# Kernel optimization log

Hardware: AMD Instinct MI355X
Metric: run time of the kernel (lower is better)

The kernel has to match this reference:

```python
import jax, jax.numpy as jnp
import numpy as np

EPS = 1e-12  # torch F.normalize eps
NUM_HEADS = 4
DT = 0.25
NUM_STEPS = 4


def _l2norm(x, axis=-1):
    n = jnp.sqrt(jnp.sum(x * x, axis=axis, keepdims=True))
    return x / jnp.maximum(n, EPS)


def setup_inputs() -> dict:
    key = jax.random.key(0)
    k0, k1, k2, k3, k4 = jax.random.split(key, 5)
    B, T, D = 4, 2048, 256
    z = jax.random.normal(k0, (B, T, D), dtype=jnp.float32)
    omega = jax.random.normal(k1, (1, 1, D), dtype=jnp.float32) * 0.1
    Wqk = jax.random.normal(k2, (2 * D, D), dtype=jnp.float32) * (1.0 / np.sqrt(D))
    Wout = jax.random.normal(k3, (D, D), dtype=jnp.float32) * (1.0 / np.sqrt(D))
    bout = jax.random.normal(k4, (D,), dtype=jnp.float32) * 0.01
    return {"z": z, "omega": omega, "Wqk": Wqk, "Wout": Wout, "bout": bout}


def _kuramoto(x, omega, Wqk, Wout, bout):
    # x: [B, T, D]
    B, T, D = x.shape
    hd = D // NUM_HEADS
    qk = x @ Wqk.T  # [B, T, 2D]
    q, k = jnp.split(qk, 2, axis=-1)
    q = _l2norm(q.reshape(B, T, NUM_HEADS, hd))  # cosine-normalized per head
    k = _l2norm(k.reshape(B, T, NUM_HEADS, hd))
    # coupling: [B, H, T, T] cosine similarity
    coupling = jnp.einsum("bqhd,bkhd->bhqk", q, k)
    # sin nonlinearity replaces softmax
    force = jnp.einsum("bhqk,bkhd->bqhd", jnp.sin(coupling), k).reshape(B, T, D)
    return omega + force @ Wout.T + bout


def reference(z, omega, Wqk, Wout, bout):
    def f(x):
        return _kuramoto(x, omega, Wqk, Wout, bout)

    x = z
    for _ in range(NUM_STEPS):
        x = _l2norm(x)
        k1 = f(x)
        k2 = f(x + DT / 2 * k1)
        k3 = f(x + DT / 2 * k2)
        k4 = f(x + DT * k3)
        x = x + DT / 6 * (k1 + 2 * k2 + 2 * k3 + k4)
    return _l2norm(x)
```

## Files before the change

### kernel.cpp

```cpp
#include <hip/hip_runtime.h>
#include <cmath>

#define NB 4
#define TT 2048
#define DD 256
#define NH 4
#define BT (NB*TT)

static constexpr float DT_ = 0.25f;

typedef _Float16 f16x8 __attribute__((ext_vector_type(8)));
typedef _Float16 f16x4 __attribute__((ext_vector_type(4)));
typedef float    f32x4 __attribute__((ext_vector_type(4)));

static constexpr size_t HSZ = (size_t)NB * NH * TT * 64;
static constexpr size_t FSZ = (size_t)BT * 256;

__device__ __forceinline__ void gload16(const void* g, void* l) {
    __builtin_amdgcn_global_load_lds(
        (const __attribute__((address_space(1))) void*)g,
        (__attribute__((address_space(3))) void*)l,
        16, 0, 0);
}

__global__ __launch_bounds__(256)
void split_weights(const float* __restrict__ Wqk, const float* __restrict__ Wout,
                   _Float16* __restrict__ WqkH, _Float16* __restrict__ WqkL,
                   _Float16* __restrict__ WoutH, _Float16* __restrict__ WoutL)
{
    const int idx = blockIdx.x * 256 + threadIdx.x;
    const float4 v = (idx < 32768) ? ((const float4*)Wqk)[idx]
                                   : ((const float4*)Wout)[idx - 32768];
    f16x4 h, l;
    h[0]=(_Float16)v.x; l[0]=(_Float16)(v.x-(float)h[0]);
    h[1]=(_Float16)v.y; l[1]=(_Float16)(v.y-(float)h[1]);
    h[2]=(_Float16)v.z; l[2]=(_Float16)(v.z-(float)h[2]);
    h[3]=(_Float16)v.w; l[3]=(_Float16)(v.w-(float)h[3]);
    if (idx < 32768) { ((f16x4*)WqkH)[idx] = h; ((f16x4*)WqkL)[idx] = l; }
    else { ((f16x4*)WoutH)[idx-32768] = h; ((f16x4*)WoutL)[idx-32768] = l; }
}

__global__ __launch_bounds__(256)
void comb_weights(const float* __restrict__ Wqk, const float* __restrict__ Wout,
                  const float* __restrict__ omega, const float* __restrict__ bout,
                  _Float16* __restrict__ WcombH, _Float16* __restrict__ WcombL,
                  float* __restrict__ qkob)
{
    __shared__ float qrow[256];
    __shared__ float pr[256];
    const int n = blockIdx.x;
    const int k = threadIdx.x;
    qrow[k] = Wqk[n * 256 + k];
    __syncthreads();
    float s = 0.f;
    for (int m = 0; m < 256; ++m) s = fmaf(qrow[m], Wout[m * 256 + k], s);
    const _Float16 h = (_Float16)s;
    WcombH[n * 256 + k] = h;
    WcombL[n * 256 + k] = (_Float16)(s - (float)h);
    pr[k] = (omega[k] + bout[k]) * qrow[k];
    __syncthreads();
    if (k == 0) {
        float t = 0.f;
        for (int i = 0; i < 256; ++i) t += pr[i];
        qkob[n] = t;
    }
}

__global__ __launch_bounds__(256)
void l2norm_rows(const float* __restrict__ src, float* __restrict__ dst,
                 _Float16* __restrict__ dstH, _Float16* __restrict__ dstL) {
    const int wave = threadIdx.x >> 6;
    const int lane = threadIdx.x & 63;
    const size_t row = (size_t)blockIdx.x * 4 + wave;
    float4 v = ((const float4*)(src + row * DD))[lane];
    float ss = v.x*v.x + v.y*v.y + v.z*v.z + v.w*v.w;
    #pragma unroll
    for (int off = 32; off; off >>= 1) ss += __shfl_xor(ss, off, 64);
    const float inv = 1.0f / fmaxf(sqrtf(ss), 1e-12f);
    v.x *= inv; v.y *= inv; v.z *= inv; v.w *= inv;
    ((float4*)(dst + row * DD))[lane] = v;
    if (dstH != nullptr) {
        f16x4 h, l;
        h[0]=(_Float16)v.x; l[0]=(_Float16)(v.x-(float)h[0]);
        h[1]=(_Float16)v.y; l[1]=(_Float16)(v.y-(float)h[1]);
        h[2]=(_Float16)v.z; l[2]=(_Float16)(v.z-(float)h[2]);
        h[3]=(_Float16)v.w; l[3]=(_Float16)(v.w-(float)h[3]);
        ((f16x4*)(dstH + row * DD))[lane] = h;
        ((f16x4*)(dstL + row * DD))[lane] = l;
    }
}

__global__ __launch_bounds__(256)
void reduce_F(const float* __restrict__ Fp, float* __restrict__ Facc,
              _Float16* __restrict__ SH, _Float16* __restrict__ SL, int faccm)
{
    const size_t idx = (size_t)blockIdx.x * 256 + threadIdx.x;
    const float4 a = ((const float4*)Fp)[idx];
    const float4 b = ((const float4*)(Fp + FSZ))[idx];
    const float4 c = ((const float4*)(Fp + 2*FSZ))[idx];
    float4 s = make_float4(a.x+b.x+c.x, a.y+b.y+c.y, a.z+b.z+c.z, a.w+b.w+c.w);
    if (faccm == 1) {
        ((float4*)Facc)[idx] = s;
    } else if (faccm == 2) {
        float4 f = ((const float4*)Facc)[idx];
        f.x += 2.f*s.x; f.y += 2.f*s.y; f.z += 2.f*s.z; f.w += 2.f*s.w;
        ((float4*)Facc)[idx] = f;
    } else {
        const float4 f = ((const float4*)Facc)[idx];
        s.x += f.x; s.y += f.y; s.z += f.z; s.w += f.w;
    }
    f16x4 h, l;
    h[0]=(_Float16)s.x; l[0]=(_Float16)(s.x-(float)h[0]);
    h[1]=(_Float16)s.y; l[1]=(_Float16)(s.y-(float)h[1]);
    h[2]=(_Float16)s.z; l[2]=(_Float16)(s.z-(float)h[2]);
    h[3]=(_Float16)s.w; l[3]=(_Float16)(s.w-(float)h[3]);
    ((f16x4*)SH)[idx] = h;
    ((f16x4*)SL)[idx] = l;
}

__global__ __launch_bounds__(256, 3)
void gemm_mfma(const _Float16* __restrict__ AH, const _Float16* __restrict__ AL,
               const _Float16* __restrict__ BH, const _Float16* __restrict__ BL,
               float* __restrict__ qkx, const float* __restrict__ qkob,
               const float* __restrict__ omega, const float* __restrict__ bout,
               const float* __restrict__ xin, float* __restrict__ xout,
               _Float16* __restrict__ Qhi, _Float16* __restrict__ Qlo,
               _Float16* __restrict__ Khi, _Float16* __restrict__ Klo,
               _Float16* __restrict__ KtrH,
               int mode, float cc)
{
    __shared__ _Float16 Ah[128 * 64];
    __shared__ _Float16 Al[128 * 64];
    __shared__ _Float16 Bh[64 * 64];
    __shared__ _Float16 Bl[64 * 64];
    const int m0 = blockIdx.x * 128, n0 = blockIdx.y * 64;
    const int t  = threadIdx.x;
    const int w  = t >> 6;
    const int l  = t & 63;
    const int lr = l & 15;
    const int lq = l >> 4;
    const int m7 = lr & 7;
    const int rr = l >> 3;
    const int cg = ((l & 7) ^ rr) * 8;

    f32x4 acc[2][4];
    #pragma unroll
    for (int s = 0; s < 2; ++s)
        #pragma unroll
        for (int nt = 0; nt < 4; ++nt) acc[s][nt] = (f32x4){0.f,0.f,0.f,0.f};

    for (int kc = 0; kc < 4; ++kc) {
        const int k0 = kc * 64;
        __syncthreads();
        #pragma unroll
        for (int a = 0; a < 4; ++a) {
            const int rg = 8*w + 32*a;
            gload16(AH + (size_t)(m0 + rg + rr) * 256 + k0 + cg, &Ah[rg * 64]);
            gload16(AL + (size_t)(m0 + rg + rr) * 256 + k0 + cg, &Al[rg * 64]);
            if (a < 2) {
                gload16(BH + (size_t)(n0 + rg + rr) * 256 + k0 + cg, &Bh[rg * 64]);
                gload16(BL + (size_t)(n0 + rg + rr) * 256 + k0 + cg, &Bl[rg * 64]);
            }
        }
        __syncthreads();
        #pragma unroll
        for (int c = 0; c < 2; ++c) {
            const int xo = (((4*c + lq) ^ m7) << 4);
            f16x8 ah[2], al[2], bh[4], bl[4];
            #pragma unroll
            for (int s = 0; s < 2; ++s) {
                ah[s] = *(const f16x8*)((const char*)Ah + (32*w + 16*s + lr) * 128 + xo);
                al[s] = *(const f16x8*)((const char*)Al + (32*w + 16*s + lr) * 128 + xo);
            }
            #pragma unroll
            for (int nt = 0; nt < 4; ++nt) {
                bh[nt] = *(const f16x8*)((const char*)Bh + (16*nt + lr) * 128 + xo);
                bl[nt] = *(const f16x8*)((const char*)Bl + (16*nt + lr) * 128 + xo);
            }
            #pragma unroll
            for (int s = 0; s < 2; ++s)
                #pragma unroll
                for (int nt = 0; nt < 4; ++nt) {
                    acc[s][nt] = __builtin_amdgcn_mfma_f32_16x16x32_f16(ah[s], bh[nt], acc[s][nt], 0, 0, 0);
                    acc[s][nt] = __builtin_amdgcn_mfma_f32_16x16x32_f16(ah[s], bl[nt], acc[s][nt], 0, 0, 0);
                    acc[s][nt] = __builtin_amdgcn_mfma_f32_16x16x32_f16(al[s], bh[nt], acc[s][nt], 0, 0, 0);
                }
        }
    }

    if (mode == 2) {
        #pragma unroll
        for (int s = 0; s < 2; ++s) {
            const int row0 = m0 + 32*w + 16*s + 4*lq;
            #pragma unroll
            for (int nt = 0; nt < 4; ++nt) {
                const int col = n0 + 16*nt + lr;
                const float ob = omega[col] + bout[col];
                #pragma unroll
                for (int r = 0; r < 4; ++r) {
                    const size_t off = (size_t)(row0 + r) * 256 + col;
                    xout[off] = xin[off] + (DT_ / 6.0f) * acc[s][nt][r] + DT_ * ob;
                }
            }
        }
    } else {
        float val[2][4][4];
        #pragma unroll
        for (int s = 0; s < 2; ++s) {
            const int row0 = m0 + 32*w + 16*s + 4*lq;
            #pragma unroll
            for (int nt = 0; nt < 4; ++nt) {
                const int col = n0 + 16*nt + lr;
                #pragma unroll
                for (int r = 0; r < 4; ++r) {
                    const size_t qo = (size_t)(row0 + r) * 512 + col;
                    if (mode == 0) {
                        val[s][nt][r] = acc[s][nt][r];
                        qkx[qo] = acc[s][nt][r];
                    } else {
                        val[s][nt][r] = qkx[qo] + cc * (acc[s][nt][r] + qkob[col]);
                    }
                }
            }
        }
        float ss[2][4];
        #pragma unroll
        for (int s = 0; s < 2; ++s)
            #pragma unroll
            for (int r = 0; r < 4; ++r) {
                float v = 0.f;
                #pragma unroll
                for (int nt = 0; nt < 4; ++nt) v += val[s][nt][r] * val[s][nt][r];
                ss[s][r] = v;
            }
        #pragma unroll
        for (int off = 1; off < 16; off <<= 1)
            #pragma unroll
            for (int s = 0; s < 2; ++s)
                #pragma unroll
                for (int r = 0; r < 4; ++r)
                    ss[s][r] += __shfl_xor(ss[s][r], off, 64);
        const int  b    = m0 >> 11;
        const int  h    = (n0 >> 6) & 3;
        const bool is_k = (n0 >= 256);
        const size_t bhi = (size_t)b * NH + h;
        _Float16* dhi = (is_k ? Khi : Qhi) + bhi * (size_t)TT * 64;
        _Float16* dlo = (is_k ? Klo : Qlo) + bhi * (size_t)TT * 64;
        const int mloc = m0 & (TT - 1);
        #pragma unroll
        for (int s = 0; s < 2; ++s) {
            const int r0 = 32*w + 16*s + 4*lq;
            float inv[4];
            #pragma unroll
            for (int r = 0; r < 4; ++r) inv[r] = 1.0f / fmaxf(sqrtf(ss[s][r]), 1e-12f);
            #pragma unroll
            for (int nt = 0; nt < 4; ++nt) {
                const int d = 16*nt + lr;
                f16x4 hv, lv;
                #pragma unroll
                for (int r = 0; r < 4; ++r) {
                    const float v2 = val[s][nt][r] * inv[r];
                    hv[r] = (_Float16)v2;
                    lv[r] = (_Float16)(v2 - (float)hv[r]);
                    dhi[(size_t)(mloc + r0 + r) * 64 + d] = hv[r];
                    dlo[(size_t)(mloc + r0 + r) * 64 + d] = lv[r];
                }
                if (is_k) {
                    const size_t tb = bhi * (size_t)64 * TT + (size_t)d * TT + mloc + r0;
                    *(f16x4*)(KtrH + tb) = hv;
                }
            }
        }
    }
}

__global__ __launch_bounds__(256, 4)
void kuramoto_attn(const _Float16* __restrict__ Qhi, const _Float16* __restrict__ Qlo,
                   const _Float16* __restrict__ Khi, const _Float16* __restrict__ Klo,
                   const _Float16* __restrict__ KtrH,
                   float* __restrict__ Fp)
{
    __shared__ _Float16 KjH[64 * 64];
    __shared__ _Float16 KjL[64 * 64];
    __shared__ _Float16 KdH[64 * 64];
    __shared__ _Float16 Pw[4][2][16 * 64];
    const int bh = blockIdx.z;
    const int b  = bh >> 2, h = bh & 3;
    const size_t base  = (size_t)bh * TT * 64;
    const size_t tbase = (size_t)bh * 64 * TT;
    const int t0 = blockIdx.y * 11;
    const int tn = (blockIdx.y == 2) ? 10 : 11;
    float* Fout = Fp + (size_t)blockIdx.y * FSZ;
    const int t = threadIdx.x;
    const int w = t >> 6;
    const int l = t & 63;
    const int lr = l & 15;
    const int lq = l >> 4;
    const int i0 = blockIdx.x * 128 + w * 32;
    const int m7 = lr & 7;
    const int x0 = ((lq ^ m7) << 4);
    const int x1 = (((lq + 4) ^ m7) << 4);
    const int rr = l >> 3;
    const int cg = ((l & 7) ^ rr) * 8;

    const _Float16* gKh = Khi  + base  + (size_t)(8*w + rr) * 64 + cg;
    const _Float16* gKl = Klo  + base  + (size_t)(8*w + rr) * 64 + cg;
    const _Float16* gKd = KtrH + tbase + (size_t)(8*w + rr) * TT + cg;
    _Float16* lKh = &KjH[(8*w) * 64];
    _Float16* lKl = &KjL[(8*w) * 64];
    _Float16* lKd = &KdH[(8*w) * 64];

    f16x8 qh[2][2], ql[2][2];
    #pragma unroll
    for (int s = 0; s < 2; ++s) {
        const size_t qoff = base + (size_t)(i0 + 16*s + lr) * 64 + lq * 8;
        qh[s][0] = *(const f16x8*)(Qhi + qoff);
        qh[s][1] = *(const f16x8*)(Qhi + qoff + 32);
        ql[s][0] = *(const f16x8*)(Qlo + qoff);
        ql[s][1] = *(const f16x8*)(Qlo + qoff + 32);
    }

    f32x4 Facc[2][4];
    #pragma unroll
    for (int s = 0; s < 2; ++s)
        #pragma unroll
        for (int nt = 0; nt < 4; ++nt) Facc[s][nt] = (f32x4){0.f, 0.f, 0.f, 0.f};

    for (int tt = 0; tt < tn; ++tt) {
        const int j0 = (t0 + tt) * 64;
        __syncthreads();
        gload16(gKh + (size_t)j0 * 64,           lKh);
        gload16(gKh + (size_t)j0 * 64 + 32 * 64, lKh + 32 * 64);
        gload16(gKl + (size_t)j0 * 64,           lKl);
        gload16(gKl + (size_t)j0 * 64 + 32 * 64, lKl + 32 * 64);
        gload16(gKd + j0,                        lKd);
        gload16(gKd + j0 + (size_t)32 * TT,      lKd + 32 * 64);
        __syncthreads();
        #pragma unroll
        for (int nt = 0; nt < 4; ++nt) {
            const int rb = (16*nt + lr) * 128;
            f16x8 kh0 = *(const f16x8*)((const char*)KjH + rb + x0);
            f16x8 kh1 = *(const f16x8*)((const char*)KjH + rb + x1);
            f16x8 kl0 = *(const f16x8*)((const char*)KjL + rb + x0);
            f16x8 kl1 = *(const f16x8*)((const char*)KjL + rb + x1);
            #pragma unroll
            for (int s = 0; s < 2; ++s) {
                f32x4 a = (f32x4){0.f, 0.f, 0.f, 0.f};
                __builtin_amdgcn_s_setprio(1);
                a = __builtin_amdgcn_mfma_f32_16x16x32_f16(kh0, qh[s][0], a, 0, 0, 0);
                a = __builtin_amdgcn_mfma_f32_16x16x32_f16(kh1, qh[s][1], a, 0, 0, 0);
                a = __builtin_amdgcn_mfma_f32_16x16x32_f16(kl0, qh[s][0], a, 0, 0, 0);
                a = __builtin_amdgcn_mfma_f32_16x16x32_f16(kl1, qh[s][1], a, 0, 0, 0);
                a = __builtin_amdgcn_mfma_f32_16x16x32_f16(kh0, ql[s][0], a, 0, 0, 0);
                a = __builtin_amdgcn_mfma_f32_16x16x32_f16(kh1, ql[s][1], a, 0, 0, 0);
                __builtin_amdgcn_s_setprio(0);
                f16x4 pv;
                #pragma unroll
                for (int r = 0; r < 4; ++r) pv[r] = (_Float16)__sinf(a[r]);
                *(f16x4*)((char*)&Pw[w][s][0] + lr * 128
                          + (((2*nt + (lq >> 1)) ^ m7) << 4) + ((lq & 1) << 3)) = pv;
            }
        }
        f16x8 ph[2][2];
        #pragma unroll
        for (int s = 0; s < 2; ++s) {
            ph[s][0] = *(const f16x8*)((const char*)&Pw[w][s][0] + lr * 128 + x0);
            ph[s][1] = *(const f16x8*)((const char*)&Pw[w][s][0] + lr * 128 + x1);
        }
        #pragma unroll
        for (int nt = 0; nt < 4; ++nt) {
            const int rb = (16*nt + lr) * 128;
            f16x8 kh0 = *(const f16x8*)((const char*)KdH + rb + x0);
            f16x8 kh1 = *(const f16x8*)((const char*)KdH + rb + x1);
            __builtin_amdgcn_s_setprio(1);
            #pragma unroll
            for (int s = 0; s < 2; ++s) {
                Facc[s][nt] = __builtin_amdgcn_mfma_f32_16x16x32_f16(ph[s][0], kh0, Facc[s][nt], 0, 0, 0);
                Facc[s][nt] = __builtin_amdgcn_mfma_f32_16x16x32_f16(ph[s][1], kh1, Facc[s][nt], 0, 0, 0);
            }
            __builtin_amdgcn_s_setprio(0);
        }
    }
    #pragma unroll
    for (int s = 0; s < 2; ++s) {
        float* fo = Fout + ((size_t)b * TT + i0 + 16*s + 4*lq) * 256 + h * 64 + lr;
        #pragma unroll
        for (int nt = 0; nt < 4; ++nt)
            #pragma unroll
            for (int r = 0; r < 4; ++r)
                fo[(size_t)r * 256 + nt * 16] = Facc[s][nt][r];
    }
}

extern "C" void kernel_launch(void* const* d_in, const int* in_sizes, int n_in,
                              void* d_out, int out_size, void* d_ws, size_t ws_size,
                              hipStream_t stream) {
    const float* z     = (const float*)d_in[0];
    const float* omega = (const float*)d_in[1];
    const float* Wqk   = (const float*)d_in[2];
    const float* Wout  = (const float*)d_in[3];
    const float* bout  = (const float*)d_in[4];

    float* x    = (float*)d_ws;
    float* Facc = x + FSZ;
    float* Fp   = Facc + FSZ;
    float* qkx  = Fp + 3 * FSZ;
    float* qkob = qkx + (size_t)BT * 512;
    _Float16* xsH  = (_Float16*)(qkob + 512);
    _Float16* xsL  = xsH  + FSZ;
    _Float16* Qhi  = xsL  + FSZ;
    _Float16* Qlo  = Qhi  + HSZ;
    _Float16* Khi  = Qlo  + HSZ;
    _Float16* Klo  = Khi  + HSZ;
    _Float16* KtrH = Klo  + HSZ;
    _Float16* WqkH = KtrH + HSZ;
    _Float16* WqkL = WqkH + (size_t)512 * 256;
    _Float16* WoutH= WqkL + (size_t)512 * 256;
    _Float16* WoutL= WoutH + (size_t)256 * 256;
    _Float16* WcombH = WoutL + (size_t)256 * 256;
    _Float16* WcombL = WcombH + (size_t)512 * 256;

    split_weights<<<192, 256, 0, stream>>>(Wqk, Wout, WqkH, WqkL, WoutH, WoutL);
    comb_weights<<<512, 256, 0, stream>>>(Wqk, Wout, omega, bout, WcombH, WcombL, qkob);

    for (int step = 0; step < 4; ++step) {
        l2norm_rows<<<BT / 4, 256, 0, stream>>>(step == 0 ? z : x, x, xsH, xsL);
        gemm_mfma<<<dim3(BT / 128, 8), 256, 0, stream>>>(
            xsH, xsL, WqkH, WqkL, qkx, nullptr,
            nullptr, nullptr, nullptr, nullptr,
            Qhi, Qlo, Khi, Klo, KtrH, 0, 0.f);
        kuramoto_attn<<<dim3(TT / 128, 3, NB * NH), 256, 0, stream>>>(
            Qhi, Qlo, Khi, Klo, KtrH, Fp);
        for (int s = 1; s <= 3; ++s) {
            const float cs = (s == 3) ? 0.25f : 0.125f;
            reduce_F<<<2048, 256, 0, stream>>>(Fp, Facc, xsH, xsL, (s == 1) ? 1 : 2);
            gemm_mfma<<<dim3(BT / 128, 8), 256, 0, stream>>>(
                xsH, xsL, WcombH, WcombL, qkx, qkob,
                nullptr, nullptr, nullptr, nullptr,
                Qhi, Qlo, Khi, Klo, KtrH, 1, cs);
            kuramoto_attn<<<dim3(TT / 128, 3, NB * NH), 256, 0, stream>>>(
                Qhi, Qlo, Khi, Klo, KtrH, Fp);
        }
        reduce_F<<<2048, 256, 0, stream>>>(Fp, Facc, xsH, xsL, 3);
        gemm_mfma<<<dim3(BT / 128, 4), 256, 0, stream>>>(
            xsH, xsL, WoutH, WoutL, nullptr, nullptr,
            omega, bout, x, x,
            nullptr, nullptr, nullptr, nullptr, nullptr, 2, 0.f);
    }
    l2norm_rows<<<BT / 4, 256, 0, stream>>>(x, (float*)d_out, nullptr, nullptr);
}
```

Measured before the change: 1.164 ms.

## Double-buffer K tiles in attention, load Klo from global, reorder grid

Rewrites the attention kernel's K-tile loop to double-buffer the high-part K and transposed K tiles in LDS. It prefetches the next tile with async global-to-LDS loads while the current one is computed, replacing the two full syncthreads per iteration with waitcnt plus barrier. The low-part K is now read straight from global into registers instead of going through LDS, which frees shared memory for the second buffer. The grid axes are swapped so blocks sharing a head launch adjacently, meant to improve L2 reuse. Occupancy hint drops from 4 to 3 blocks per CU, and the per-thread global Klo loads may add latency and register pressure.

```diff
diff --git a/kernel.cpp b/kernel.cpp
--- a/kernel.cpp
+++ b/kernel.cpp
@@ -274,17 +274,16 @@
     }
 }
 
-__global__ __launch_bounds__(256, 4)
+__global__ __launch_bounds__(256, 3)
 void kuramoto_attn(const _Float16* __restrict__ Qhi, const _Float16* __restrict__ Qlo,
                    const _Float16* __restrict__ Khi, const _Float16* __restrict__ Klo,
                    const _Float16* __restrict__ KtrH,
                    float* __restrict__ Fp)
 {
-    __shared__ _Float16 KjH[64 * 64];
-    __shared__ _Float16 KjL[64 * 64];
-    __shared__ _Float16 KdH[64 * 64];
+    __shared__ _Float16 KjH[2][64 * 64];
+    __shared__ _Float16 KdH[2][64 * 64];
     __shared__ _Float16 Pw[4][2][16 * 64];
-    const int bh = blockIdx.z;
+    const int bh = blockIdx.x;
     const int b  = bh >> 2, h = bh & 3;
     const size_t base  = (size_t)bh * TT * 64;
     const size_t tbase = (size_t)bh * 64 * TT;
@@ -296,7 +295,7 @@
     const int l = t & 63;
     const int lr = l & 15;
     const int lq = l >> 4;
-    const int i0 = blockIdx.x * 128 + w * 32;
+    const int i0 = blockIdx.z * 128 + w * 32;
     const int m7 = lr & 7;
     const int x0 = ((lq ^ m7) << 4);
     const int x1 = (((lq + 4) ^ m7) << 4);
@@ -304,11 +303,7 @@
     const int cg = ((l & 7) ^ rr) * 8;
 
     const _Float16* gKh = Khi  + base  + (size_t)(8*w + rr) * 64 + cg;
-    const _Float16* gKl = Klo  + base  + (size_t)(8*w + rr) * 64 + cg;
     const _Float16* gKd = KtrH + tbase + (size_t)(8*w + rr) * TT + cg;
-    _Float16* lKh = &KjH[(8*w) * 64];
-    _Float16* lKl = &KjL[(8*w) * 64];
-    _Float16* lKd = &KdH[(8*w) * 64];
 
     f16x8 qh[2][2], ql[2][2];
     #pragma unroll
@@ -326,31 +321,48 @@
         #pragma unroll
         for (int nt = 0; nt < 4; ++nt) Facc[s][nt] = (f32x4){0.f, 0.f, 0.f, 0.f};
 
+#define STAGE_TILE(TTi, BB) do { \
+        const int j0_ = (t0 + (TTi)) * 64; \
+        gload16(gKh + (size_t)j0_ * 64,           &KjH[BB][(8*w) * 64]); \
+        gload16(gKh + (size_t)j0_ * 64 + 32 * 64, &KjH[BB][(8*w) * 64 + 32 * 64]); \
+        gload16(gKd + j0_,                        &KdH[BB][(8*w) * 64]); \
+        gload16(gKd + j0_ + (size_t)32 * TT,      &KdH[BB][(8*w) * 64 + 32 * 64]); \
+    } while (0)
+
+    STAGE_TILE(0, 0);
+
     for (int tt = 0; tt < tn; ++tt) {
+        const int cur = tt & 1;
+        if (tt + 1 < tn) {
+            STAGE_TILE(tt + 1, cur ^ 1);
+            asm volatile("s_waitcnt vmcnt(4)" ::: "memory");
+        } else {
+            asm volatile("s_waitcnt vmcnt(0)" ::: "memory");
+        }
+        __builtin_amdgcn_s_barrier();
+        asm volatile("" ::: "memory");
+
         const int j0 = (t0 + tt) * 64;
-        __syncthreads();
-        gload16(gKh + (size_t)j0 * 64,           lKh);
-        gload16(gKh + (size_t)j0 * 64 + 32 * 64, lKh + 32 * 64);
-        gload16(gKl + (size_t)j0 * 64,           lKl);
-        gload16(gKl + (size_t)j0 * 64 + 32 * 64, lKl + 32 * 64);
-        gload16(gKd + j0,                        lKd);
-        gload16(gKd + j0 + (size_t)32 * TT,      lKd + 32 * 64);
-        __syncthreads();
+        f16x8 klA[4], klB[4];
+        #pragma unroll
+        for (int nt = 0; nt < 4; ++nt) {
+            const _Float16* kp = Klo + base + (size_t)(j0 + 16*nt + lr) * 64 + 8*lq;
+            klA[nt] = *(const f16x8*)kp;
+            klB[nt] = *(const f16x8*)(kp + 32);
+        }
         #pragma unroll
         for (int nt = 0; nt < 4; ++nt) {
             const int rb = (16*nt + lr) * 128;
-            f16x8 kh0 = *(const f16x8*)((const char*)KjH + rb + x0);
-            f16x8 kh1 = *(const f16x8*)((const char*)KjH + rb + x1);
-            f16x8 kl0 = *(const f16x8*)((const char*)KjL + rb + x0);
-            f16x8 kl1 = *(const f16x8*)((const char*)KjL + rb + x1);
+            f16x8 kh0 = *(const f16x8*)((const char*)&KjH[cur][0] + rb + x0);
+            f16x8 kh1 = *(const f16x8*)((const char*)&KjH[cur][0] + rb + x1);
             #pragma unroll
             for (int s = 0; s < 2; ++s) {
                 f32x4 a = (f32x4){0.f, 0.f, 0.f, 0.f};
                 __builtin_amdgcn_s_setprio(1);
                 a = __builtin_amdgcn_mfma_f32_16x16x32_f16(kh0, qh[s][0], a, 0, 0, 0);
                 a = __builtin_amdgcn_mfma_f32_16x16x32_f16(kh1, qh[s][1], a, 0, 0, 0);
-                a = __builtin_amdgcn_mfma_f32_16x16x32_f16(kl0, qh[s][0], a, 0, 0, 0);
-                a = __builtin_amdgcn_mfma_f32_16x16x32_f16(kl1, qh[s][1], a, 0, 0, 0);
+                a = __builtin_amdgcn_mfma_f32_16x16x32_f16(klA[nt], qh[s][0], a, 0, 0, 0);
+                a = __builtin_amdgcn_mfma_f32_16x16x32_f16(klB[nt], qh[s][1], a, 0, 0, 0);
                 a = __builtin_amdgcn_mfma_f32_16x16x32_f16(kh0, ql[s][0], a, 0, 0, 0);
                 a = __builtin_amdgcn_mfma_f32_16x16x32_f16(kh1, ql[s][1], a, 0, 0, 0);
                 __builtin_amdgcn_s_setprio(0);
@@ -370,8 +382,8 @@
         #pragma unroll
         for (int nt = 0; nt < 4; ++nt) {
             const int rb = (16*nt + lr) * 128;
-            f16x8 kh0 = *(const f16x8*)((const char*)KdH + rb + x0);
-            f16x8 kh1 = *(const f16x8*)((const char*)KdH + rb + x1);
+            f16x8 kh0 = *(const f16x8*)((const char*)&KdH[cur][0] + rb + x0);
+            f16x8 kh1 = *(const f16x8*)((const char*)&KdH[cur][0] + rb + x1);
             __builtin_amdgcn_s_setprio(1);
             #pragma unroll
             for (int s = 0; s < 2; ++s) {
@@ -380,7 +392,11 @@
             }
             __builtin_amdgcn_s_setprio(0);
         }
-    }
+        __builtin_amdgcn_s_barrier();
+        asm volatile("" ::: "memory");
+    }
+#undef STAGE_TILE
+
     #pragma unroll
     for (int s = 0; s < 2; ++s) {
         float* fo = Fout + ((size_t)b * TT + i0 + 16*s + 4*lq) * 256 + h * 64 + lr;
@@ -429,7 +445,7 @@
             xsH, xsL, WqkH, WqkL, qkx, nullptr,
             nullptr, nullptr, nullptr, nullptr,
             Qhi, Qlo, Khi, Klo, KtrH, 0, 0.f);
-        kuramoto_attn<<<dim3(TT / 128, 3, NB * NH), 256, 0, stream>>>(
+        kuramoto_attn<<<dim3(NB * NH, 3, TT / 128), 256, 0, stream>>>(
             Qhi, Qlo, Khi, Klo, KtrH, Fp);
         for (int s = 1; s <= 3; ++s) {
             const float cs = (s == 3) ? 0.25f : 0.125f;
@@ -438,7 +454,7 @@
                 xsH, xsL, WcombH, WcombL, qkx, qkob,
                 nullptr, nullptr, nullptr, nullptr,
                 Qhi, Qlo, Khi, Klo, KtrH, 1, cs);
-            kuramoto_attn<<<dim3(TT / 128, 3, NB * NH), 256, 0, stream>>>(
+            kuramoto_attn<<<dim3(NB * NH, 3, TT / 128), 256, 0, stream>>>(
                 Qhi, Qlo, Khi, Klo, KtrH, Fp);
         }
         reduce_F<<<2048, 256, 0, stream>>>(Fp, Facc, xsH, xsL, 3);
```

New measurement: 1.242 ms. +6.7%, slower.

## Register-prefetch next K tile in attention and reorder grid for head-major dispatch

Applied to the files above, without the earlier changes.

Replaces the direct global-to-LDS async loads, which sat between two barriers, with register prefetch. The next K tile is loaded into registers while the current tile is computed, then written to swizzled LDS at the top of the next iteration, so global latency can overlap with MFMA and sin work. The grid is also reordered so blockIdx.x walks batch-heads, which changes how blocks sharing K tiles are scheduled together and may affect L2 reuse. The occupancy hint drops from 4 to 3 blocks per SM, giving more registers for the prefetch buffers at the cost of fewer resident waves.

```diff
diff --git a/kernel.cpp b/kernel.cpp
--- a/kernel.cpp
+++ b/kernel.cpp
@@ -274,7 +274,7 @@
     }
 }
 
-__global__ __launch_bounds__(256, 4)
+__global__ __launch_bounds__(256, 3)
 void kuramoto_attn(const _Float16* __restrict__ Qhi, const _Float16* __restrict__ Qlo,
                    const _Float16* __restrict__ Khi, const _Float16* __restrict__ Klo,
                    const _Float16* __restrict__ KtrH,
@@ -284,7 +284,7 @@
     __shared__ _Float16 KjL[64 * 64];
     __shared__ _Float16 KdH[64 * 64];
     __shared__ _Float16 Pw[4][2][16 * 64];
-    const int bh = blockIdx.z;
+    const int bh = blockIdx.x;
     const int b  = bh >> 2, h = bh & 3;
     const size_t base  = (size_t)bh * TT * 64;
     const size_t tbase = (size_t)bh * 64 * TT;
@@ -296,19 +296,14 @@
     const int l = t & 63;
     const int lr = l & 15;
     const int lq = l >> 4;
-    const int i0 = blockIdx.x * 128 + w * 32;
+    const int i0 = blockIdx.z * 128 + w * 32;
     const int m7 = lr & 7;
     const int x0 = ((lq ^ m7) << 4);
     const int x1 = (((lq + 4) ^ m7) << 4);
     const int rr = l >> 3;
-    const int cg = ((l & 7) ^ rr) * 8;
-
-    const _Float16* gKh = Khi  + base  + (size_t)(8*w + rr) * 64 + cg;
-    const _Float16* gKl = Klo  + base  + (size_t)(8*w + rr) * 64 + cg;
-    const _Float16* gKd = KtrH + tbase + (size_t)(8*w + rr) * TT + cg;
-    _Float16* lKh = &KjH[(8*w) * 64];
-    _Float16* lKl = &KjL[(8*w) * 64];
-    _Float16* lKd = &KdH[(8*w) * 64];
+    const int lc8 = (l & 7) * 8;
+    const int sw = ((l & 7) ^ rr) * 8;
+    const int rg = 8 * w + rr;
 
     f16x8 qh[2][2], ql[2][2];
     #pragma unroll
@@ -326,16 +321,31 @@
         #pragma unroll
         for (int nt = 0; nt < 4; ++nt) Facc[s][nt] = (f32x4){0.f, 0.f, 0.f, 0.f};
 
+    uint4 gA0, gA1, gB0, gB1, gC0, gC1;
+#define GLOAD(TTi) do { \
+        const int j0_ = (t0 + (TTi)) * 64; \
+        gA0 = *(const uint4*)(Khi  + base  + (size_t)(j0_ + rg)      * 64 + lc8); \
+        gA1 = *(const uint4*)(Khi  + base  + (size_t)(j0_ + rg + 32) * 64 + lc8); \
+        gB0 = *(const uint4*)(Klo  + base  + (size_t)(j0_ + rg)      * 64 + lc8); \
+        gB1 = *(const uint4*)(Klo  + base  + (size_t)(j0_ + rg + 32) * 64 + lc8); \
+        gC0 = *(const uint4*)(KtrH + tbase + (size_t)rg        * TT + j0_ + lc8); \
+        gC1 = *(const uint4*)(KtrH + tbase + (size_t)(rg + 32) * TT + j0_ + lc8); \
+    } while (0)
+
+    GLOAD(0);
+
     for (int tt = 0; tt < tn; ++tt) {
-        const int j0 = (t0 + tt) * 64;
-        __syncthreads();
-        gload16(gKh + (size_t)j0 * 64,           lKh);
-        gload16(gKh + (size_t)j0 * 64 + 32 * 64, lKh + 32 * 64);
-        gload16(gKl + (size_t)j0 * 64,           lKl);
-        gload16(gKl + (size_t)j0 * 64 + 32 * 64, lKl + 32 * 64);
-        gload16(gKd + j0,                        lKd);
-        gload16(gKd + j0 + (size_t)32 * TT,      lKd + 32 * 64);
-        __syncthreads();
+        *(uint4*)&KjH[rg * 64 + sw]        = gA0;
+        *(uint4*)&KjH[(rg + 32) * 64 + sw] = gA1;
+        *(uint4*)&KjL[rg * 64 + sw]        = gB0;
+        *(uint4*)&KjL[(rg + 32) * 64 + sw] = gB1;
+        *(uint4*)&KdH[rg * 64 + sw]        = gC0;
+        *(uint4*)&KdH[(rg + 32) * 64 + sw] = gC1;
+        if (tt + 1 < tn) GLOAD(tt + 1);
+        asm volatile("s_waitcnt lgkmcnt(0)" ::: "memory");
+        __builtin_amdgcn_s_barrier();
+        asm volatile("" ::: "memory");
+
         #pragma unroll
         for (int nt = 0; nt < 4; ++nt) {
             const int rb = (16*nt + lr) * 128;
@@ -357,15 +367,15 @@
                 f16x4 pv;
                 #pragma unroll
                 for (int r = 0; r < 4; ++r) pv[r] = (_Float16)__sinf(a[r]);
-                *(f16x4*)((char*)&Pw[w][s][0] + lr * 128
+                *(f16x4*)((char*)&Pw[w][0][0] + ((int)sizeof(_Float16))*0 + s * 2048 + lr * 128
                           + (((2*nt + (lq >> 1)) ^ m7) << 4) + ((lq & 1) << 3)) = pv;
             }
         }
         f16x8 ph[2][2];
         #pragma unroll
         for (int s = 0; s < 2; ++s) {
-            ph[s][0] = *(const f16x8*)((const char*)&Pw[w][s][0] + lr * 128 + x0);
-            ph[s][1] = *(const f16x8*)((const char*)&Pw[w][s][0] + lr * 128 + x1);
+            ph[s][0] = *(const f16x8*)((const char*)&Pw[w][0][0] + s * 2048 + lr * 128 + x0);
+            ph[s][1] = *(const f16x8*)((const char*)&Pw[w][0][0] + s * 2048 + lr * 128 + x1);
         }
         #pragma unroll
         for (int nt = 0; nt < 4; ++nt) {
@@ -380,7 +390,11 @@
             }
             __builtin_amdgcn_s_setprio(0);
         }
-    }
+        __builtin_amdgcn_s_barrier();
+        asm volatile("" ::: "memory");
+    }
+#undef GLOAD
+
     #pragma unroll
     for (int s = 0; s < 2; ++s) {
         float* fo = Fout + ((size_t)b * TT + i0 + 16*s + 4*lq) * 256 + h * 64 + lr;
@@ -429,7 +443,7 @@
             xsH, xsL, WqkH, WqkL, qkx, nullptr,
             nullptr, nullptr, nullptr, nullptr,
             Qhi, Qlo, Khi, Klo, KtrH, 0, 0.f);
-        kuramoto_attn<<<dim3(TT / 128, 3, NB * NH), 256, 0, stream>>>(
+        kuramoto_attn<<<dim3(NB * NH, 3, TT / 128), 256, 0, stream>>>(
             Qhi, Qlo, Khi, Klo, KtrH, Fp);
         for (int s = 1; s <= 3; ++s) {
             const float cs = (s == 3) ? 0.25f : 0.125f;
@@ -438,7 +452,7 @@
                 xsH, xsL, WcombH, WcombL, qkx, qkob,
                 nullptr, nullptr, nullptr, nullptr,
                 Qhi, Qlo, Khi, Klo, KtrH, 1, cs);
-            kuramoto_attn<<<dim3(TT / 128, 3, NB * NH), 256, 0, stream>>>(
+            kuramoto_attn<<<dim3(NB * NH, 3, TT / 128), 256, 0, stream>>>(
                 Qhi, Qlo, Khi, Klo, KtrH, Fp);
         }
         reduce_F<<<2048, 256, 0, stream>>>(Fp, Facc, xsH, xsL, 3);
```

New measurement: 1.161 ms. Within noise of the previous version (-0.3%).
